# Kernel optimization log

Measured on AMD Instinct MI355X. Metric: run time of the kernel, lower is better.

Reference implementation:

```python
import jax, jax.numpy as jnp
import numpy as np

N_NODES = 20000
N_EDGES = 320000


def gcn_conv(x, W, b, src, dst, n_nodes):
    """PyG GCNConv: add self-loops, symmetric D^-1/2 (A+I) D^-1/2 normalization,
    linear transform then normalized scatter-add aggregation, plus bias."""
    x = x @ W  # [N, out]
    loop = jnp.arange(n_nodes, dtype=src.dtype)
    s = jnp.concatenate([src, loop])  # [E+N]
    d = jnp.concatenate([dst, loop])
    # degree of destination nodes (edge weight = 1), including self-loops
    deg = jax.ops.segment_sum(jnp.ones_like(d, dtype=x.dtype), d, num_segments=n_nodes)
    dinv = jnp.where(deg > 0, jax.lax.rsqrt(deg), 0.0)
    norm = dinv[s] * dinv[d]  # [E+N]
    msg = x[s] * norm[:, None]  # gather + scale, [E+N, out]
    out = jax.ops.segment_sum(msg, d, num_segments=n_nodes)  # scatter-add
    return out + b


def setup_inputs() -> dict:
    key = jax.random.key(0)
    ks = jax.random.split(key, 8)
    x = jax.random.normal(ks[0], (N_NODES, 10), dtype=jnp.float32)
    edge_index = jax.random.randint(ks[1], (2, N_EDGES), 0, N_NODES, dtype=jnp.int32)
    # Glorot-ish init for weights, zero bias (as in PyG defaults)
    def glorot(k, shape):
        lim = float(np.sqrt(6.0 / (shape[0] + shape[1])))
        return jax.random.uniform(k, shape, jnp.float32, -lim, lim)
    return {
        "x": x,
        "edge_index": edge_index,
        "W1": glorot(ks[2], (10, 256)),
        "b1": jnp.zeros((256,), jnp.float32),
        "W2": glorot(ks[3], (256, 128)),
        "b2": jnp.zeros((128,), jnp.float32),
        "W3": glorot(ks[4], (128, 1)),
        "b3": jnp.zeros((1,), jnp.float32),
    }


def reference(x, edge_index, W1, b1, W2, b2, W3, b3):
    src, dst = edge_index[0], edge_index[1]
    n = x.shape[0]
    h = jax.nn.relu(gcn_conv(x, W1, b1, src, dst, n))
    h = jax.nn.relu(gcn_conv(h, W2, b2, src, dst, n))
    out = gcn_conv(h, W3, b3, src, dst, n)
    return out.squeeze(-1)  # [N]
```

## Files before the change

### kernel.cpp

```cpp
#include <hip/hip_runtime.h>


constexpr int NN  = 20000;
constexpr int NE  = 320000;
constexpr int F0  = 10;
constexpr int F1  = 256;
constexpr int F2  = 128;
constexpr int MB  = 16;
constexpr int CAP = 64;


__global__ void k_fill(const int* __restrict__ src, const int* __restrict__ dst,
                       int* cursor, int* __restrict__ col) {
  int e = blockIdx.x * 256 + threadIdx.x;
  if (e >= NE) return;
  const int d = dst[e], s = src[e];
  const int pos = atomicAdd(&cursor[d], 1) & (CAP - 1);
  col[d * CAP + pos] = s;
}


__global__ __launch_bounds__(256) void k_gemm12(
    const float* __restrict__ x, const int* __restrict__ cursor,
    const int* __restrict__ col, const float* __restrict__ W1,
    const float* __restrict__ b1, const float* __restrict__ W2,
    float* __restrict__ t2s) {
  __shared__ float alds[MB * F0];
  __shared__ float h1[MB][F1 + 4];
  __shared__ float w2lds[32 * F2];
  const int tid = threadIdx.x;
  const int n0 = blockIdx.x * MB;
  {
    const int m = tid >> 4;
    const int f = tid & 15;
    if (f < F0) {
      const int n = n0 + m;
      const int deg = cursor[n];
      const int base = n * CAP;
      const float di = rsqrtf((float)(deg + 1));
      float acc = x[n * F0 + f] * di;
      int k = 0;
      for (; k + 3 < deg; k += 4) {
        const int s0 = col[base + k],     s1 = col[base + k + 1];
        const int s2 = col[base + k + 2], s3 = col[base + k + 3];
        const float d0 = rsqrtf((float)(cursor[s0] + 1));
        const float d1 = rsqrtf((float)(cursor[s1] + 1));
        const float d2 = rsqrtf((float)(cursor[s2] + 1));
        const float d3 = rsqrtf((float)(cursor[s3] + 1));
        acc += x[s0 * F0 + f] * d0 + x[s1 * F0 + f] * d1 +
               x[s2 * F0 + f] * d2 + x[s3 * F0 + f] * d3;
      }
      for (; k < deg; ++k) {
        const int s = col[base + k];
        acc += x[s * F0 + f] * rsqrtf((float)(cursor[s] + 1));
      }
      alds[m * F0 + f] = di * acc;
    }
  }
  float4 pf0 = *((const float4*)W2 + tid);
  float4 pf1 = *((const float4*)W2 + tid + 256);
  float4 pf2 = *((const float4*)W2 + tid + 512);
  float4 pf3 = *((const float4*)W2 + tid + 768);
  __syncthreads();
  {
    const int c = tid;
    float w1r[F0];
#pragma unroll
    for (int k = 0; k < F0; ++k) w1r[k] = W1[k * F1 + c];
    const float bb = b1[c];
#pragma unroll
    for (int m = 0; m < MB; ++m) {
      float acc = bb;
#pragma unroll
      for (int k = 0; k < F0; ++k) acc += alds[m * F0 + k] * w1r[k];
      h1[m][c] = fmaxf(acc, 0.f);
    }
  }
  const int cg_ = tid & 31;
  const int m0 = (tid >> 5) * 2;
  float a00 = 0.f, a01 = 0.f, a02 = 0.f, a03 = 0.f;
  float a10 = 0.f, a11 = 0.f, a12 = 0.f, a13 = 0.f;
#define FMA4(av, bv, vw)                                            \
  a00 += (av) * (vw).x; a01 += (av) * (vw).y;                       \
  a02 += (av) * (vw).z; a03 += (av) * (vw).w;                       \
  a10 += (bv) * (vw).x; a11 += (bv) * (vw).y;                       \
  a12 += (bv) * (vw).z; a13 += (bv) * (vw).w;
  for (int kc = 0; kc < F1 / 32; ++kc) {
    __syncthreads();
    {
      float4* ldst = (float4*)w2lds;
      ldst[tid] = pf0;
      ldst[tid + 256] = pf1;
      ldst[tid + 512] = pf2;
      ldst[tid + 768] = pf3;
    }
    __syncthreads();
    if (kc + 1 < F1 / 32) {
      const float4* gnext = (const float4*)(W2 + (kc + 1) * 32 * F2);
      pf0 = gnext[tid];
      pf1 = gnext[tid + 256];
      pf2 = gnext[tid + 512];
      pf3 = gnext[tid + 768];
    }
#pragma unroll
    for (int kk = 0; kk < 32; kk += 4) {
      const int k = kc * 32 + kk;
      const float4 ha = *(const float4*)&h1[m0][k];
      const float4 hb = *(const float4*)&h1[m0 + 1][k];
      const float4 w0 = *(const float4*)&w2lds[(kk + 0) * F2 + cg_ * 4];
      const float4 w1v = *(const float4*)&w2lds[(kk + 1) * F2 + cg_ * 4];
      const float4 w2v = *(const float4*)&w2lds[(kk + 2) * F2 + cg_ * 4];
      const float4 w3v = *(const float4*)&w2lds[(kk + 3) * F2 + cg_ * 4];
      FMA4(ha.x, hb.x, w0);
      FMA4(ha.y, hb.y, w1v);
      FMA4(ha.z, hb.z, w2v);
      FMA4(ha.w, hb.w, w3v);
    }
  }
#undef FMA4
  const float d0 = rsqrtf((float)(cursor[n0 + m0] + 1));
  const float d1 = rsqrtf((float)(cursor[n0 + m0 + 1] + 1));
  *(float4*)&t2s[(size_t)(n0 + m0) * F2 + cg_ * 4] =
      make_float4(a00 * d0, a01 * d0, a02 * d0, a03 * d0);
  *(float4*)&t2s[(size_t)(n0 + m0 + 1) * F2 + cg_ * 4] =
      make_float4(a10 * d1, a11 * d1, a12 * d1, a13 * d1);
}


__global__ __launch_bounds__(256) void k_agg2(
    const float* __restrict__ t2s, const int* __restrict__ cursor,
    const int* __restrict__ col, const float* __restrict__ b2,
    const float* __restrict__ W3, float* __restrict__ t3s) {
  const int wave = (blockIdx.x * 256 + threadIdx.x) >> 6;
  const int lane = threadIdx.x & 63;
  const int half = lane >> 5;
  const int li   = lane & 31;
  const int n    = wave * 2 + half;
  if (n >= NN) return;
  const int deg = cursor[n];
  const int base = n * CAP;
  const int fx = li * 4;
  const float4 vs = *(const float4*)&t2s[(size_t)n * F2 + fx];
  float a0 = vs.x, a1 = vs.y, a2 = vs.z, a3 = vs.w;
  int k = 0;
  for (; k + 7 < deg; k += 8) {
    const int s0 = col[base + k],     s1 = col[base + k + 1];
    const int s2 = col[base + k + 2], s3 = col[base + k + 3];
    const int s4 = col[base + k + 4], s5 = col[base + k + 5];
    const int s6 = col[base + k + 6], s7 = col[base + k + 7];
    const float4 v0 = *(const float4*)&t2s[(size_t)s0 * F2 + fx];
    const float4 v1 = *(const float4*)&t2s[(size_t)s1 * F2 + fx];
    const float4 v2 = *(const float4*)&t2s[(size_t)s2 * F2 + fx];
    const float4 v3 = *(const float4*)&t2s[(size_t)s3 * F2 + fx];
    const float4 v4 = *(const float4*)&t2s[(size_t)s4 * F2 + fx];
    const float4 v5 = *(const float4*)&t2s[(size_t)s5 * F2 + fx];
    const float4 v6 = *(const float4*)&t2s[(size_t)s6 * F2 + fx];
    const float4 v7 = *(const float4*)&t2s[(size_t)s7 * F2 + fx];
    a0 += ((v0.x + v1.x) + (v2.x + v3.x)) + ((v4.x + v5.x) + (v6.x + v7.x));
    a1 += ((v0.y + v1.y) + (v2.y + v3.y)) + ((v4.y + v5.y) + (v6.y + v7.y));
    a2 += ((v0.z + v1.z) + (v2.z + v3.z)) + ((v4.z + v5.z) + (v6.z + v7.z));
    a3 += ((v0.w + v1.w) + (v2.w + v3.w)) + ((v4.w + v5.w) + (v6.w + v7.w));
  }
  for (; k + 3 < deg; k += 4) {
    const int s0 = col[base + k],     s1 = col[base + k + 1];
    const int s2 = col[base + k + 2], s3 = col[base + k + 3];
    const float4 v0 = *(const float4*)&t2s[(size_t)s0 * F2 + fx];
    const float4 v1 = *(const float4*)&t2s[(size_t)s1 * F2 + fx];
    const float4 v2 = *(const float4*)&t2s[(size_t)s2 * F2 + fx];
    const float4 v3 = *(const float4*)&t2s[(size_t)s3 * F2 + fx];
    a0 += (v0.x + v1.x) + (v2.x + v3.x);
    a1 += (v0.y + v1.y) + (v2.y + v3.y);
    a2 += (v0.z + v1.z) + (v2.z + v3.z);
    a3 += (v0.w + v1.w) + (v2.w + v3.w);
  }
  for (; k < deg; ++k) {
    const float4 v = *(const float4*)&t2s[(size_t)col[base + k] * F2 + fx];
    a0 += v.x; a1 += v.y; a2 += v.z; a3 += v.w;
  }
  const float di = rsqrtf((float)(deg + 1));
  const float4 bb = *(const float4*)&b2[fx];
  const float4 w3 = *(const float4*)&W3[fx];
  const float h0 = fmaxf(di * a0 + bb.x, 0.f);
  const float h1 = fmaxf(di * a1 + bb.y, 0.f);
  const float h2 = fmaxf(di * a2 + bb.z, 0.f);
  const float h3 = fmaxf(di * a3 + bb.w, 0.f);
  float p = (h0 * w3.x + h1 * w3.y) + (h2 * w3.z + h3 * w3.w);
#pragma unroll
  for (int off = 16; off > 0; off >>= 1) p += __shfl_down(p, off);
  if (li == 0) t3s[n] = di * p;
}


__global__ void k_agg3(const float* __restrict__ t3s, const int* __restrict__ cursor,
                       const int* __restrict__ col, const float* __restrict__ b3,
                       float* __restrict__ out) {
  int n = blockIdx.x * 256 + threadIdx.x;
  if (n >= NN) return;
  const int deg = cursor[n];
  const int base = n * CAP;
  float acc = t3s[n];
  int k = 0;
  for (; k + 7 < deg; k += 8)
    acc += ((t3s[col[base + k]] + t3s[col[base + k + 1]]) +
            (t3s[col[base + k + 2]] + t3s[col[base + k + 3]])) +
           ((t3s[col[base + k + 4]] + t3s[col[base + k + 5]]) +
            (t3s[col[base + k + 6]] + t3s[col[base + k + 7]]));
  for (; k < deg; ++k) acc += t3s[col[base + k]];
  out[n] = rsqrtf((float)(deg + 1)) * acc + b3[0];
}

extern "C" void kernel_launch(void* const* d_in, const int* in_sizes, int n_in,
                              void* d_out, int out_size, void* d_ws, size_t ws_size,
                              hipStream_t stream) {
  const float* x = (const float*)d_in[0];
  const int* ei = (const int*)d_in[1];
  const int* srcv = ei;
  const int* dstv = ei + NE;
  const float* W1 = (const float*)d_in[2];
  const float* b1 = (const float*)d_in[3];
  const float* W2 = (const float*)d_in[4];
  const float* b2 = (const float*)d_in[5];
  const float* W3 = (const float*)d_in[6];
  const float* b3 = (const float*)d_in[7];
  float* out = (float*)d_out;

  char* w = (char*)d_ws;
  auto alloc = [&](size_t bytes) -> void* {
    void* p = (void*)w;
    w += (bytes + 255) & ~(size_t)255;
    return p;
  };
  int*   cursor = (int*)  alloc(NN * 4);
  int*   col    = (int*)  alloc((size_t)NN * CAP * 4);
  float* t2s    = (float*)alloc((size_t)NN * F2 * 4);
  float* t3s    = (float*)alloc(NN * 4);

  (void)hipMemsetAsync(cursor, 0, NN * 4, stream);
  k_fill<<<(NE + 255) / 256, 256, 0, stream>>>(srcv, dstv, cursor, col);
  k_gemm12<<<NN / MB, 256, 0, stream>>>(x, cursor, col, W1, b1, W2, t2s);
  k_agg2<<<NN / 8, 256, 0, stream>>>(t2s, cursor, col, b2, W3, t3s);
  k_agg3<<<(NN + 255) / 256, 256, 0, stream>>>(t3s, cursor, col, b3, out);
}
```

Measured before the change: 148.4 us.

## Split K across lane groups in layer-2 GEMM with shuffle reduction

Reorganizes the per-block 16x256 by 256x128 GEMM in k_gemm12 so that each wave covers 8 rows and 16 column groups. The four 16-lane groups within a wave each take an 8-wide slice of every 32-wide K chunk, and the partial sums are combined with cross-lane shuffles. The aim is to cut LDS traffic per FMA: each W2 float4 is reused across 8 rows and h1 reads become broadcasts, where before each thread did a 2x4 register tile. The cost is 32 accumulator registers per thread and a shuffle reduction epilogue in which most of the reduced values are thrown away.

New measurement: 159.5 us. 1.07x slower.

```diff
diff --git a/kernel.cpp b/kernel.cpp
--- a/kernel.cpp
+++ b/kernel.cpp
@@ -76,15 +76,16 @@
       h1[m][c] = fmaxf(acc, 0.f);
     }
   }
-  const int cg_ = tid & 31;
-  const int m0 = (tid >> 5) * 2;
-  float a00 = 0.f, a01 = 0.f, a02 = 0.f, a03 = 0.f;
-  float a10 = 0.f, a11 = 0.f, a12 = 0.f, a13 = 0.f;
-#define FMA4(av, bv, vw)                                            \
-  a00 += (av) * (vw).x; a01 += (av) * (vw).y;                       \
-  a02 += (av) * (vw).z; a03 += (av) * (vw).w;                       \
-  a10 += (bv) * (vw).x; a11 += (bv) * (vw).y;                       \
-  a12 += (bv) * (vw).z; a13 += (bv) * (vw).w;
+  const int lane = tid & 63;
+  const int wv   = tid >> 6;
+  const int kg   = lane >> 4;
+  const int ctl  = lane & 15;
+  const int mBase = (wv >> 1) * 8;
+  const int ct    = ((wv & 1) << 4) + ctl;
+  float4 acc[8];
+#pragma unroll
+  for (int i = 0; i < 8; ++i) acc[i] = make_float4(0.f, 0.f, 0.f, 0.f);
+
   for (int kc = 0; kc < F1 / 32; ++kc) {
     __syncthreads();
     {
@@ -103,27 +104,48 @@
       pf3 = gnext[tid + 768];
     }
 #pragma unroll
-    for (int kk = 0; kk < 32; kk += 4) {
-      const int k = kc * 32 + kk;
-      const float4 ha = *(const float4*)&h1[m0][k];
-      const float4 hb = *(const float4*)&h1[m0 + 1][k];
-      const float4 w0 = *(const float4*)&w2lds[(kk + 0) * F2 + cg_ * 4];
-      const float4 w1v = *(const float4*)&w2lds[(kk + 1) * F2 + cg_ * 4];
-      const float4 w2v = *(const float4*)&w2lds[(kk + 2) * F2 + cg_ * 4];
-      const float4 w3v = *(const float4*)&w2lds[(kk + 3) * F2 + cg_ * 4];
-      FMA4(ha.x, hb.x, w0);
-      FMA4(ha.y, hb.y, w1v);
-      FMA4(ha.z, hb.z, w2v);
-      FMA4(ha.w, hb.w, w3v);
-    }
-  }
-#undef FMA4
-  const float d0 = rsqrtf((float)(cursor[n0 + m0] + 1));
-  const float d1 = rsqrtf((float)(cursor[n0 + m0 + 1] + 1));
-  *(float4*)&t2s[(size_t)(n0 + m0) * F2 + cg_ * 4] =
-      make_float4(a00 * d0, a01 * d0, a02 * d0, a03 * d0);
-  *(float4*)&t2s[(size_t)(n0 + m0 + 1) * F2 + cg_ * 4] =
-      make_float4(a10 * d1, a11 * d1, a12 * d1, a13 * d1);
+    for (int kk = 0; kk < 8; kk += 4) {
+      const int kl = (kg << 3) + kk;
+      const int kb = (kc << 5) + kl;
+      const float4 w0v = *(const float4*)&w2lds[(kl + 0) * F2 + (ct << 2)];
+      const float4 w1v = *(const float4*)&w2lds[(kl + 1) * F2 + (ct << 2)];
+      const float4 w2v = *(const float4*)&w2lds[(kl + 2) * F2 + (ct << 2)];
+      const float4 w3v = *(const float4*)&w2lds[(kl + 3) * F2 + (ct << 2)];
+#pragma unroll
+      for (int i = 0; i < 8; ++i) {
+        const float4 hv = *(const float4*)&h1[mBase + i][kb];
+        acc[i].x += hv.x * w0v.x + hv.y * w1v.x + hv.z * w2v.x + hv.w * w3v.x;
+        acc[i].y += hv.x * w0v.y + hv.y * w1v.y + hv.z * w2v.y + hv.w * w3v.y;
+        acc[i].z += hv.x * w0v.z + hv.y * w1v.z + hv.z * w2v.z + hv.w * w3v.z;
+        acc[i].w += hv.x * w0v.w + hv.y * w1v.w + hv.z * w2v.w + hv.w * w3v.w;
+      }
+    }
+  }
+#pragma unroll
+  for (int i = 0; i < 8; ++i) {
+    acc[i].x += __shfl_xor(acc[i].x, 16);
+    acc[i].y += __shfl_xor(acc[i].y, 16);
+    acc[i].z += __shfl_xor(acc[i].z, 16);
+    acc[i].w += __shfl_xor(acc[i].w, 16);
+    acc[i].x += __shfl_xor(acc[i].x, 32);
+    acc[i].y += __shfl_xor(acc[i].y, 32);
+    acc[i].z += __shfl_xor(acc[i].z, 32);
+    acc[i].w += __shfl_xor(acc[i].w, 32);
+  }
+  float4 r0 = make_float4(0.f, 0.f, 0.f, 0.f), r1 = r0;
+#pragma unroll
+  for (int i = 0; i < 8; ++i) {
+    if ((i >> 1) == kg) {
+      if (i & 1) r1 = acc[i]; else r0 = acc[i];
+    }
+  }
+  const int m = mBase + (kg << 1);
+  const float d0 = rsqrtf((float)(cursor[n0 + m] + 1));
+  const float d1 = rsqrtf((float)(cursor[n0 + m + 1] + 1));
+  *(float4*)&t2s[(size_t)(n0 + m) * F2 + (ct << 2)] =
+      make_float4(r0.x * d0, r0.y * d0, r0.z * d0, r0.w * d0);
+  *(float4*)&t2s[(size_t)(n0 + m + 1) * F2 + (ct << 2)] =
+      make_float4(r1.x * d1, r1.y * d1, r1.z * d1, r1.w * d1);
 }
 
 
```
